# Kernel optimization log

Hardware: AMD Instinct MI355X
Metric: run time of the kernel (lower is better)

The kernel has to match this reference:

```python
import jax, jax.numpy as jnp
import numpy as np

BH, BW = 64, 64            # base model input (block) size
STRIDE = 16                # block // 4, per WindowObjectDetector.predict
N_CLASSES = 10
THRESH = 0.7


def _extract_patches(x, bh, bw, stride):
    # x: [1, H, W, 3] -> [R, C, bh, bw, 3], VALID padding (tf.image.extract_patches)
    H, W = x.shape[1], x.shape[2]
    R = (H - bh) // stride + 1
    C = (W - bw) // stride + 1
    r = (jnp.arange(R) * stride)[:, None] + jnp.arange(bh)   # [R, bh]
    c = (jnp.arange(C) * stride)[:, None] + jnp.arange(bw)   # [C, bw]
    p = x[0][r]                 # [R, bh, W, 3]
    p = p[:, :, c]              # [R, bh, C, bw, 3]
    return jnp.transpose(p, (0, 2, 1, 3, 4))  # [R, C, bh, bw, 3]


def _connected_components(mask):
    # mask: bool [K, R, C]; 4-connectivity min-label propagation.
    K, R, C = mask.shape
    BIG = jnp.int32(R * C + 2)
    seed = (jnp.arange(R * C, dtype=jnp.int32).reshape(R, C) + 1)[None]  # [1,R,C]
    lbl0 = jnp.where(mask, seed, 0)

    def prop(l):
        xm = jnp.where(mask, l, BIG)
        n = xm
        n = jnp.minimum(n, jnp.pad(xm, ((0, 0), (1, 0), (0, 0)), constant_values=R * C + 2)[:, :R, :])
        n = jnp.minimum(n, jnp.pad(xm, ((0, 0), (0, 1), (0, 0)), constant_values=R * C + 2)[:, 1:, :])
        n = jnp.minimum(n, jnp.pad(xm, ((0, 0), (0, 0), (1, 0)), constant_values=R * C + 2)[:, :, :C])
        n = jnp.minimum(n, jnp.pad(xm, ((0, 0), (0, 0), (0, 1)), constant_values=R * C + 2)[:, :, 1:])
        return jnp.where(mask, n, 0)

    def cond(carry):
        prev, cur = carry
        return jnp.any(prev != cur)

    def body(carry):
        _, cur = carry
        return cur, prop(cur)

    _, lbl = jax.lax.while_loop(cond, body, (lbl0, prop(lbl0)))
    return lbl  # [K, R, C] int32, 0 = background


def _boxes_from_labels(labels):
    # labels: [K, R, C] -> padded boxes [K, R*C+1, 4] (rowmin-1, colmin-1, rowmax+1, colmax+1)
    K, R, C = labels.shape
    S = R * C + 1
    rr = jnp.repeat(jnp.arange(R, dtype=jnp.int32), C)  # [R*C]
    cc = jnp.tile(jnp.arange(C, dtype=jnp.int32), R)
    flat = labels.reshape(K, R * C)

    def per_class(lbl_k):
        rmin = jax.ops.segment_min(rr, lbl_k, num_segments=S)
        rmax = jax.ops.segment_max(rr, lbl_k, num_segments=S)
        cmin = jax.ops.segment_min(cc, lbl_k, num_segments=S)
        cmax = jax.ops.segment_max(cc, lbl_k, num_segments=S)
        cnt = jax.ops.segment_sum(jnp.ones_like(lbl_k), lbl_k, num_segments=S)
        valid = (cnt > 0) & (jnp.arange(S) > 0)
        box = jnp.stack([rmin - 1, cmin - 1, rmax + 1, cmax + 1], axis=-1)
        box = jnp.where(valid[:, None], box, -1)
        return box, valid

    return jax.vmap(per_class)(flat)


def setup_inputs() -> dict:
    key = jax.random.key(0)
    k1, k2, k3 = jax.random.split(key, 3)
    inputs = jax.random.uniform(k1, (1, 1024, 1024, 3), dtype=jnp.float32)
    W = jax.random.normal(k2, (BH * BW * 3, N_CLASSES), dtype=jnp.float32) * 0.02
    b = jax.random.normal(k3, (N_CLASSES,), dtype=jnp.float32)
    return {"inputs": inputs, "W": W, "b": b}


def reference(inputs, W, b):
    # Windowing: extract 64x64 patches with stride 16 (image divisible by 64 -> no resize)
    patches = _extract_patches(inputs, BH, BW, STRIDE)          # [R, C, 64, 64, 3]
    R, C = patches.shape[0], patches.shape[1]
    flat = patches.reshape(R * C, BH * BW * 3)
    logits = flat @ W + b                                        # base model
    prob = jax.nn.softmax(logits, axis=1).reshape(R, C, N_CLASSES)
    mask = prob > THRESH                                         # [R, C, K]
    # tf transposes before/after connected_components (4-connectivity is symmetric)
    labels = _connected_components(jnp.transpose(mask, (2, 0, 1)))  # [K, R, C]
    labels = jnp.transpose(labels, (1, 2, 0))                    # [R, C, K]
    boxes, valid = _boxes_from_labels(jnp.transpose(labels, (2, 0, 1)))
    return prob, labels, boxes, valid
```

## Files before the change

### kernel.cpp

```cpp
#include <hip/hip_runtime.h>
#include <math.h>

#define RG 61
#define CG 61
#define NP 3721
#define NSEG 3722
#define NCLS 10
#define THRESHV 0.7f
#define BIGI 0x3FFFFFFF

#define NKQ 16
#define NBLK (RG*NKQ)
#define CHS 51
#define ROWF (64*CHS)
#define PROW 640

typedef __attribute__((address_space(4))) const float cfl;

__global__ __launch_bounds__(256, 3) void wod_logits_part(
    const float* __restrict__ img,
    const float* __restrict__ W,
    float* __restrict__ part)
{
    __shared__ float simg[4 * ROWF];
    const int tid = threadIdx.x;
    const int o  = (blockIdx.x & 7) * 122 + (blockIdx.x >> 3);
    const int r  = o >> 4;
    const int kq = o & 15;
    const int R0 = 16 * r + 4 * kq;

    for (int u = tid; u < 3072; u += 256) {
        const int row = u / 768;
        const int v   = u - row * 768;
        const int p0  = v * 4;
        const float4 x4 = *(const float4*)(img + (size_t)(R0 + row) * 3072 + p0);
        const int ch = p0 / 48;
        float* d = simg + row * ROWF + ch * CHS + (p0 - ch * 48);
        d[0] = x4.x; d[1] = x4.y; d[2] = x4.z; d[3] = x4.w;
    }
    __syncthreads();

    const int wv = __builtin_amdgcn_readfirstlane(tid >> 6);
    const int c  = tid & 63;
    const int cx = c > 60 ? 60 : c;
    const int wr = 4 * kq + wv;

    const cfl*   wbase = (const cfl*)W + wr * 1920;
    const float* srow  = simg + wv * ROWF + cx * CHS;

    float acc[NCLS];
    #pragma unroll
    for (int k = 0; k < NCLS; ++k) acc[k] = 0.f;

    #pragma unroll 1
    for (int cc2 = 0; cc2 < 4; ++cc2) {
        const float* sch = srow + cc2 * CHS;
        const cfl*   wch = wbase + cc2 * 480;
        #pragma unroll
        for (int q6 = 0; q6 < 6; ++q6) {
            #pragma unroll
            for (int j = 0; j < 4; ++j) {
                const int le = q6 * 8 + 2 * j;
                const float xx = sch[le];
                const float xy = sch[le + 1];
                const cfl* wp = wch + le * 10;
                float w_[20];
                #pragma unroll
                for (int k = 0; k < 20; ++k) w_[k] = wp[k];
                #pragma unroll
                for (int k = 0; k < NCLS; ++k) {
                    acc[k] = fmaf(xx, w_[k],      acc[k]);
                    acc[k] = fmaf(xy, w_[k + 10], acc[k]);
                }
            }
        }
    }

    __syncthreads();
    float* scratch = simg;
    {
        float* sc = scratch + wv * PROW + c * 10;
        #pragma unroll
        for (int k = 0; k < NCLS; ++k) sc[k] = acc[k];
    }
    __syncthreads();
    for (int t = tid; t < PROW; t += 256)
        part[(size_t)o * PROW + t] = scratch[t] + scratch[PROW + t]
                                   + scratch[2 * PROW + t] + scratch[3 * PROW + t];
}

__global__ __launch_bounds__(256) void wod_reduce(
    const float* __restrict__ part,
    const float* __restrict__ bias,
    float* __restrict__ out_prob,
    int* __restrict__ mask)
{
    __shared__ float lg[PROW];
    const int r   = blockIdx.x;
    const int tid = threadIdx.x;
    const float* pb = part + (size_t)r * NKQ * PROW;

    for (int t = tid; t < PROW; t += 256) {
        float s = bias[t - (t / 10) * 10];
        #pragma unroll 4
        for (int kq = 0; kq < NKQ; ++kq) s += pb[kq * PROW + t];
        lg[t] = s;
    }
    __syncthreads();

    for (int c = tid; c < CG; c += 256) {
        float l[NCLS];
        #pragma unroll
        for (int k = 0; k < NCLS; ++k) l[k] = lg[c * 10 + k];
        float m = -1e30f;
        #pragma unroll
        for (int k = 0; k < NCLS; ++k) m = fmaxf(m, l[k]);
        float ex[NCLS], sm = 0.f;
        #pragma unroll
        for (int k = 0; k < NCLS; ++k) { ex[k] = expf(l[k] - m); sm += ex[k]; }
        const float inv = 1.f / sm;
        const int cell = r * CG + c;
        #pragma unroll
        for (int k = 0; k < NCLS; ++k) {
            const float pr = ex[k] * inv;
            out_prob[cell * 10 + k] = pr;
            mask[k * NP + cell] = (pr > THRESHV) ? 1 : 0;
        }
    }
}

__global__ __launch_bounds__(256) void wod_cc(
    const int* __restrict__ mask,
    float* __restrict__ out_lbl,
    float* __restrict__ out_box,
    float* __restrict__ out_valid)
{
    const int k = blockIdx.x;
    const int tid = threadIdx.x;
    __shared__ int lbl[NP];
    __shared__ int ext0[NSEG], ext1[NSEG];
    __shared__ int changed;

    const int* mk = mask + k * NP;
    for (int idx = tid; idx < NP; idx += 256)
        lbl[idx] = mk[idx] ? (idx + 1) : 0;
    if (tid == 0) changed = 0;
    __syncthreads();

    for (;;) {
        for (int idx = tid; idx < NP; idx += 256) {
            int v = lbl[idx];
            if (v) {
                const int rr = idx / CG;
                const int cc = idx - rr * CG;
                int best = v;
                if (rr > 0)      { int n = lbl[idx - CG]; if (n && n < best) best = n; }
                if (rr < RG - 1) { int n = lbl[idx + CG]; if (n && n < best) best = n; }
                if (cc > 0)      { int n = lbl[idx - 1];  if (n && n < best) best = n; }
                if (cc < CG - 1) { int n = lbl[idx + 1];  if (n && n < best) best = n; }
                if (best < v) { lbl[idx] = best; changed = 1; }
            }
        }
        __syncthreads();
        const bool stop = (changed == 0);
        __syncthreads();
        if (stop) break;
        if (tid == 0) changed = 0;
        __syncthreads();
    }

    for (int idx = tid; idx < NP; idx += 256)
        out_lbl[idx * NCLS + k] = (float)lbl[idx];

    float* boxk = out_box + k * NSEG * 4;
    float* valk = out_valid + k * NSEG;

    for (int s2 = tid; s2 < NSEG; s2 += 256) { ext0[s2] = BIGI; ext1[s2] = BIGI; }
    __syncthreads();
    for (int idx = tid; idx < NP; idx += 256) {
        const int v = lbl[idx];
        if (v) {
            const int rr = idx / CG, cc = idx - rr * CG;
            atomicMin(&ext0[v], rr);
            atomicMin(&ext1[v], cc);
        }
    }
    __syncthreads();
    for (int s2 = tid; s2 < NSEG; s2 += 256) {
        const bool valid = (s2 > 0) && (ext0[s2] != BIGI);
        boxk[s2 * 4 + 0] = valid ? (float)(ext0[s2] - 1) : -1.f;
        boxk[s2 * 4 + 1] = valid ? (float)(ext1[s2] - 1) : -1.f;
        valk[s2] = valid ? 1.f : 0.f;
    }
    __syncthreads();

    for (int s2 = tid; s2 < NSEG; s2 += 256) { ext0[s2] = -1; ext1[s2] = -1; }
    __syncthreads();
    for (int idx = tid; idx < NP; idx += 256) {
        const int v = lbl[idx];
        if (v) {
            const int rr = idx / CG, cc = idx - rr * CG;
            atomicMax(&ext0[v], rr);
            atomicMax(&ext1[v], cc);
        }
    }
    __syncthreads();
    for (int s2 = tid; s2 < NSEG; s2 += 256) {
        const bool valid = (s2 > 0) && (ext0[s2] >= 0);
        boxk[s2 * 4 + 2] = valid ? (float)(ext0[s2] + 1) : -1.f;
        boxk[s2 * 4 + 3] = valid ? (float)(ext1[s2] + 1) : -1.f;
    }
}

extern "C" void kernel_launch(void* const* d_in, const int* in_sizes, int n_in,
                              void* d_out, int out_size, void* d_ws, size_t ws_size,
                              hipStream_t stream) {
    (void)in_sizes; (void)n_in; (void)out_size; (void)ws_size;
    const float* img = (const float*)d_in[0];
    const float* W   = (const float*)d_in[1];
    const float* b   = (const float*)d_in[2];

    float* out       = (float*)d_out;
    float* out_prob  = out;
    float* out_lbl   = out + 37210;
    float* out_box   = out + 74420;
    float* out_valid = out + 223300;

    int*   mask = (int*)d_ws;
    float* part = (float*)((int*)d_ws + NCLS * NP);

    hipLaunchKernelGGL(wod_logits_part, dim3(NBLK), dim3(256), 0, stream,
                       img, W, part);
    hipLaunchKernelGGL(wod_reduce, dim3(RG), dim3(256), 0, stream,
                       part, b, out_prob, mask);
    hipLaunchKernelGGL(wod_cc, dim3(NCLS), dim3(256), 0, stream,
                       mask, out_lbl, out_box, out_valid);
}
```

Baseline: 48.35 us.

## Reorganize logits blocks so each weight row is reused across four output rows

Each block of the logits kernel now owns one weight row and four output rows, rather than one output row and four weight rows. Every weight chunk loaded from constant memory is applied to four image rows held in shared memory, which cuts weight load traffic per FMA. The cost is four times as many accumulators per thread, a clamp on padded rows, and a partial-sum buffer 64 deep instead of 16 deep, so the reduce kernel has to read more data.

```diff
diff --git a/kernel.cpp b/kernel.cpp
--- a/kernel.cpp
+++ b/kernel.cpp
@@ -9,11 +9,10 @@
 #define THRESHV 0.7f
 #define BIGI 0x3FFFFFFF
 
-#define NKQ 16
-#define NBLK (RG*NKQ)
 #define CHS 51
 #define ROWF (64*CHS)
 #define PROW 640
+#define NBLK 1024
 
 typedef __attribute__((address_space(4))) const float cfl;
 
@@ -24,18 +23,18 @@
 {
     __shared__ float simg[4 * ROWF];
     const int tid = threadIdx.x;
-    const int o  = (blockIdx.x & 7) * 122 + (blockIdx.x >> 3);
-    const int r  = o >> 4;
-    const int kq = o & 15;
-    const int R0 = 16 * r + 4 * kq;
+    const int o  = ((blockIdx.x & 7) << 7) + (blockIdx.x >> 3);
+    const int wr = o >> 4;
+    const int rg = o & 15;
 
     for (int u = tid; u < 3072; u += 256) {
-        const int row = u / 768;
-        const int v   = u - row * 768;
-        const int p0  = v * 4;
-        const float4 x4 = *(const float4*)(img + (size_t)(R0 + row) * 3072 + p0);
+        const int t  = u / 768;
+        const int v  = u - t * 768;
+        const int p0 = v * 4;
+        int rr = 4 * rg + t; if (rr > 60) rr = 60;
+        const float4 x4 = *(const float4*)(img + (size_t)(16 * rr + wr) * 3072 + p0);
         const int ch = p0 / 48;
-        float* d = simg + row * ROWF + ch * CHS + (p0 - ch * 48);
+        float* d = simg + t * ROWF + ch * CHS + (p0 - ch * 48);
         d[0] = x4.x; d[1] = x4.y; d[2] = x4.z; d[3] = x4.w;
     }
     __syncthreads();
@@ -43,35 +42,28 @@
     const int wv = __builtin_amdgcn_readfirstlane(tid >> 6);
     const int c  = tid & 63;
     const int cx = c > 60 ? 60 : c;
-    const int wr = 4 * kq + wv;
-
-    const cfl*   wbase = (const cfl*)W + wr * 1920;
-    const float* srow  = simg + wv * ROWF + cx * CHS;
-
-    float acc[NCLS];
+
+    const cfl*   wq = (const cfl*)W + wr * 1920 + wv * 480;
+    const float* x0 = simg + (cx + wv) * CHS;
+
+    float acc[4][NCLS];
     #pragma unroll
-    for (int k = 0; k < NCLS; ++k) acc[k] = 0.f;
-
-    #pragma unroll 1
-    for (int cc2 = 0; cc2 < 4; ++cc2) {
-        const float* sch = srow + cc2 * CHS;
-        const cfl*   wch = wbase + cc2 * 480;
-        #pragma unroll
-        for (int q6 = 0; q6 < 6; ++q6) {
+    for (int t = 0; t < 4; ++t)
+        #pragma unroll
+        for (int k = 0; k < NCLS; ++k) acc[t][k] = 0.f;
+
+    #pragma unroll
+    for (int j = 0; j < 24; ++j) {
+        float w_[20];
+        #pragma unroll
+        for (int k = 0; k < 20; ++k) w_[k] = wq[j * 20 + k];
+        #pragma unroll
+        for (int t = 0; t < 4; ++t) {
+            const float2 x = *(const float2*)(x0 + t * ROWF + 2 * j);
             #pragma unroll
-            for (int j = 0; j < 4; ++j) {
-                const int le = q6 * 8 + 2 * j;
-                const float xx = sch[le];
-                const float xy = sch[le + 1];
-                const cfl* wp = wch + le * 10;
-                float w_[20];
-                #pragma unroll
-                for (int k = 0; k < 20; ++k) w_[k] = wp[k];
-                #pragma unroll
-                for (int k = 0; k < NCLS; ++k) {
-                    acc[k] = fmaf(xx, w_[k],      acc[k]);
-                    acc[k] = fmaf(xy, w_[k + 10], acc[k]);
-                }
+            for (int k = 0; k < NCLS; ++k) {
+                acc[t][k] = fmaf(x.x, w_[k],      acc[t][k]);
+                acc[t][k] = fmaf(x.y, w_[k + 10], acc[t][k]);
             }
         }
     }
@@ -79,14 +71,23 @@
     __syncthreads();
     float* scratch = simg;
     {
-        float* sc = scratch + wv * PROW + c * 10;
-        #pragma unroll
-        for (int k = 0; k < NCLS; ++k) sc[k] = acc[k];
-    }
-    __syncthreads();
-    for (int t = tid; t < PROW; t += 256)
-        part[(size_t)o * PROW + t] = scratch[t] + scratch[PROW + t]
-                                   + scratch[2 * PROW + t] + scratch[3 * PROW + t];
+        float* sc = scratch + wv * 2560 + c * 10;
+        #pragma unroll
+        for (int t = 0; t < 4; ++t)
+            #pragma unroll
+            for (int k = 0; k < NCLS; ++k)
+                sc[t * 640 + k] = acc[t][k];
+    }
+    __syncthreads();
+    for (int u = tid; u < 2560; u += 256) {
+        const int t = u / 640, e = u - t * 640;
+        const int rr = 4 * rg + t;
+        if (rr <= 60 && e < 610) {
+            const int b = t * 640 + e;
+            part[(size_t)(rr * 64 + wr) * PROW + e] =
+                scratch[b] + scratch[2560 + b] + scratch[5120 + b] + scratch[7680 + b];
+        }
+    }
 }
 
 __global__ __launch_bounds__(256) void wod_reduce(
@@ -95,15 +96,15 @@
     float* __restrict__ out_prob,
     int* __restrict__ mask)
 {
-    __shared__ float lg[PROW];
+    __shared__ float lg[610];
     const int r   = blockIdx.x;
     const int tid = threadIdx.x;
-    const float* pb = part + (size_t)r * NKQ * PROW;
-
-    for (int t = tid; t < PROW; t += 256) {
+    const float* pb = part + (size_t)r * 64 * PROW;
+
+    for (int t = tid; t < 610; t += 256) {
         float s = bias[t - (t / 10) * 10];
-        #pragma unroll 4
-        for (int kq = 0; kq < NKQ; ++kq) s += pb[kq * PROW + t];
+        #pragma unroll 8
+        for (int wr = 0; wr < 64; ++wr) s += pb[wr * PROW + t];
         lg[t] = s;
     }
     __syncthreads();
```

After: 93.58 us. 93.5% more time.
